# Kernel optimization log

Hardware: AMD Instinct MI355X
Metric: run time of the kernel (lower is better)

Reference implementation:

```python
import jax, jax.numpy as jnp
import numpy as np

B, S, V, E, H = 64, 512, 32000, 512, 1024


def setup_inputs() -> dict:
    key = jax.random.key(0)
    ks = jax.random.split(key, 8)
    s = 1.0 / np.sqrt(H).astype(np.float32)
    x = jax.random.randint(ks[0], (B, S), 0, V)  # token ids
    h0 = jnp.zeros((B, H), jnp.float32)
    c0 = jnp.zeros((B, H), jnp.float32)
    emb = jax.random.normal(ks[1], (V, E), jnp.float32) * 0.02
    W_ih = jax.random.uniform(ks[2], (4 * H, E), jnp.float32, -s, s)
    W_hh = jax.random.uniform(ks[3], (4 * H, H), jnp.float32, -s, s)
    b_ih = jax.random.uniform(ks[4], (4 * H,), jnp.float32, -s, s)
    b_hh = jax.random.uniform(ks[5], (4 * H,), jnp.float32, -s, s)
    fc_w = jax.random.uniform(ks[6], (1, H), jnp.float32, -s, s)
    fc_b = jax.random.uniform(ks[7], (1,), jnp.float32, -s, s)
    return {"x": x, "h0": h0, "c0": c0, "emb": emb, "W_ih": W_ih,
            "W_hh": W_hh, "b_ih": b_ih, "b_hh": b_hh, "fc_w": fc_w, "fc_b": fc_b}


def reference(x, h0, c0, emb, W_ih, W_hh, b_ih, b_hh, fc_w, fc_b):
    embeds = emb[x]                      # [B, S, E]
    xs = jnp.swapaxes(embeds, 0, 1)      # [S, B, E] for scan over time
    # precompute input projections for all timesteps in one big GEMM
    xproj = jnp.einsum('sbe,ge->sbg', xs, W_ih) + b_ih  # [S, B, 4H]

    def step(carry, xg):
        h, c = carry
        gates = xg + h @ W_hh.T + b_hh   # [B, 4H], torch LSTMCell gate order i,f,g,o
        i, f, g, o = jnp.split(gates, 4, axis=-1)
        c2 = jax.nn.sigmoid(f) * c + jax.nn.sigmoid(i) * jnp.tanh(g)
        h2 = jax.nn.sigmoid(o) * jnp.tanh(c2)
        return (h2, c2), None

    (h, c), _ = jax.lax.scan(step, (h0, c0), xproj)
    # dropout is identity in eval mode
    out = h @ fc_w.T + fc_b              # [B, 1]
    sig = jax.nn.sigmoid(out)
    sig_out = sig.reshape(x.shape[0], -1)[:, -1]  # [B]
    return (sig_out, h, c)
```

## Files before the change

kernel.cpp:

```cpp
#include <hip/hip_runtime.h>

typedef unsigned short u16;
typedef unsigned int   u32;

typedef __bf16 bf16x8 __attribute__((ext_vector_type(8)));
typedef float  f32x4  __attribute__((ext_vector_type(4)));

#define NB   64
#define NS   512
#define NE   512
#define NH   1024
#define NK   1536
#define NV   32000

#define WPKF_BYTES  12582912u
#define HFRAG_BYTES 262144u
#define AEMBF_BYTES 33554432u
#define BSUM_BYTES  16384u
#define BAR_BYTES   32768u

__device__ __forceinline__ u16 f2bf(float f) {
    u32 u = __builtin_bit_cast(u32, f);
    u += 0x7fffu + ((u >> 16) & 1u);
    return (u16)(u >> 16);
}
__device__ __forceinline__ bf16x8 pack8(float4 a, float4 b) {
    union { u16 u[8]; bf16x8 v; } o;
    o.u[0]=f2bf(a.x); o.u[1]=f2bf(a.y); o.u[2]=f2bf(a.z); o.u[3]=f2bf(a.w);
    o.u[4]=f2bf(b.x); o.u[5]=f2bf(b.y); o.u[6]=f2bf(b.z); o.u[7]=f2bf(b.w);
    return o.v;
}
__device__ __forceinline__ float sigf(float x) {
    return __frcp_rn(1.0f + __expf(-x));
}
__device__ __forceinline__ float tanhf_fast(float x) {
    return 1.0f - 2.0f * __frcp_rn(__expf(2.0f * x) + 1.0f);
}
__device__ __forceinline__ int clamptok(int t) {
    return t < 0 ? 0 : (t >= NV ? NV - 1 : t);
}

__global__ void init_state(const float* __restrict__ h0,
                           const float* __restrict__ c0,
                           float* __restrict__ out) {
    int i = blockIdx.x * 256 + threadIdx.x;
    float* out_h = out + 64;
    float* out_c = out + 64 + NB * NH;
    ((float4*)out_h)[i] = ((const float4*)h0)[i];
    ((float4*)out_c)[i] = ((const float4*)c0)[i];
}

__global__ void init_hfrag(const float* __restrict__ h0,
                           u16* __restrict__ hfrag0) {
    int blk = blockIdx.x, lane = threadIdx.x;
    int bg = blk >> 5, kt = blk & 31;
    int n16 = lane & 15, quad = lane >> 4;
    int b = bg * 16 + n16;
    int k = kt * 32 + quad * 8;
    const float* src = h0 + (size_t)b * NH + k;
    union { bf16x8 v; uint4 q; } o;
    o.v = pack8(*(const float4*)src, *(const float4*)(src + 4));
    *(uint4*)(hfrag0 + ((size_t)blk * 64 + lane) * 8) = o.q;
}

__global__ void prep_wfrag(const float* __restrict__ Wih,
                           const float* __restrict__ Whh,
                           u16* __restrict__ wpkf) {
    int blk = blockIdx.x, t = threadIdx.x;
    int cg = blk / 48, kt = blk % 48;
    int f = t >> 6, lane = t & 63;
    int n16 = lane & 15, quad = lane >> 4;
    int nl = f * 16 + n16;
    int j = (nl >> 3) * NH + cg * 8 + (nl & 7);
    int k = kt * 32 + quad * 8;
    const float* src = (k < NH) ? (Whh + (size_t)j * NH + k)
                                : (Wih + (size_t)j * NE + (k - NH));
    union { bf16x8 v; uint4 q; } o;
    o.v = pack8(*(const float4*)src, *(const float4*)(src + 4));
    *(uint4*)(wpkf + (((size_t)blk * 2 + f) * 64 + lane) * 8) = o.q;
}

__global__ void prep_aembf(const int* __restrict__ x,
                           const float* __restrict__ emb,
                           u16* __restrict__ aembf) {
    int blk = blockIdx.x, t = threadIdx.x;
    int s = blk >> 2, bg = blk & 3;
#pragma unroll
    for (int i = 0; i < 4; ++i) {
        int u = t + i * 256;
        int kt16 = u >> 6, lane = u & 63;
        int n16 = lane & 15, quad = lane >> 4;
        int b = bg * 16 + n16;
        int tok = clamptok(x[b * NS + s]);
        const float* ep = emb + (size_t)tok * NE + kt16 * 32 + quad * 8;
        union { bf16x8 v; uint4 q; } o;
        o.v = pack8(*(const float4*)ep, *(const float4*)(ep + 4));
        *(uint4*)(aembf + (((size_t)blk * 16 + kt16) * 64 + lane) * 8) = o.q;
    }
}

__global__ void prep_bsum(const float* __restrict__ bih,
                          const float* __restrict__ bhh,
                          float* __restrict__ bsum,
                          unsigned* __restrict__ bar) {
    int i = blockIdx.x * 256 + threadIdx.x;
    bsum[i] = bih[i] + bhh[i];
    bar[i] = 0u;
    bar[i + 4096] = 0u;
}

template<bool EMBF>
__device__ __forceinline__ void persist_body(
    const int* __restrict__ x, const float* __restrict__ emb,
    const u16* __restrict__ wpkf, const u16* __restrict__ aembf,
    u16* __restrict__ hf0, u16* __restrict__ hf1,
    const float* __restrict__ bsum, const float* __restrict__ c0,
    float* __restrict__ cstate, float* __restrict__ out_h,
    unsigned* __restrict__ bar)
{
    const int tid  = threadIdx.x;
    const int lane = tid & 63;
    const int w    = tid >> 6;
    const int blk  = blockIdx.x;
    const int cg   = blk & 127;
    const int bgp  = blk >> 7;
    const int quad = lane >> 4;
    const int n16  = lane & 15;

    __shared__ u16   lw[48 * 2 * 64 * 8];
    __shared__ float part[4][32][36];

    {
        const uint4* src = (const uint4*)(wpkf + (size_t)cg * (48 * 2 * 64 * 8));
        uint4* dst = (uint4*)lw;
#pragma unroll
        for (int i = 0; i < 24; ++i)
            dst[i * 256 + tid] = src[i * 256 + tid];
    }

    const int mloc = tid >> 3;
    const int uu   = tid & 7;
    const int be   = bgp * 32 + mloc;
    const int je   = cg * 8 + uu;
    const float bp0 = bsum[0 * NH + je];
    const float bp1 = bsum[1 * NH + je];
    const float bp2 = bsum[2 * NH + je];
    const float bp3 = bsum[3 * NH + je];
    float c_reg = c0[(size_t)be * NH + je];

    const int kth   = cg >> 2;
    const int lane2 = (cg & 3) * 16 + (mloc & 15);
    const int bgW   = bgp * 2 + (mloc >> 4);
    const size_t hwo_base = ((size_t)(bgW * 32 + kth) * 64 + lane2) * 8;

    const int bg0 = bgp * 2, bg1 = bg0 + 1;

    unsigned* my_flag = bar + ((size_t)(bgp * 128 + cg) * 32);
    const unsigned* pf0 = bar + ((size_t)(bgp * 128 + 2 * lane + 0) * 32);
    const unsigned* pf1 = bar + ((size_t)(bgp * 128 + 2 * lane + 1) * 32);

    bf16x8 ea0[4], ea1[4];
    auto loadE = [&](int s) {
        if (EMBF) {
            const u16* e0 = aembf + ((size_t)(s * 4 + bg0) * 16) * (64 * 8);
            const u16* e1 = aembf + ((size_t)(s * 4 + bg1) * 16) * (64 * 8);
#pragma unroll
            for (int i = 0; i < 4; ++i) {
                int ke = w * 4 + i;
                ea0[i] = *(const bf16x8*)(e0 + ((size_t)ke * 64 + lane) * 8);
                ea1[i] = *(const bf16x8*)(e1 + ((size_t)ke * 64 + lane) * 8);
            }
        } else {
            int t0 = clamptok(x[(bg0 * 16 + n16) * NS + s]);
            int t1 = clamptok(x[(bg1 * 16 + n16) * NS + s]);
            const float* p0 = emb + (size_t)t0 * NE + quad * 8;
            const float* p1 = emb + (size_t)t1 * NE + quad * 8;
#pragma unroll
            for (int i = 0; i < 4; ++i) {
                int ko = (w * 4 + i) * 32;
                ea0[i] = pack8(*(const float4*)(p0 + ko), *(const float4*)(p0 + ko + 4));
                ea1[i] = pack8(*(const float4*)(p1 + ko), *(const float4*)(p1 + ko + 4));
            }
        }
    };
    loadE(0);
    __syncthreads();

#pragma unroll 1
    for (int s = 0; s < NS; ++s) {
        const u16* hb = (s & 1) ? hf1 : hf0;
        u16*       ho = (s & 1) ? hf0 : hf1;
        const u16* hb0 = hb + (size_t)(bg0 * 32) * (64 * 8);
        const u16* hb1 = hb + (size_t)(bg1 * 32) * (64 * 8);

        f32x4 acc00 = {0.f,0.f,0.f,0.f}, acc01 = {0.f,0.f,0.f,0.f};
        f32x4 acc10 = {0.f,0.f,0.f,0.f}, acc11 = {0.f,0.f,0.f,0.f};

        uint4 hv0[8], hv1[8];
#pragma unroll
        for (int i = 0; i < 8; ++i) {
            const u16* a0p = hb0 + ((size_t)((w * 8 + i) * 64 + lane)) * 8;
            const u16* a1p = hb1 + ((size_t)((w * 8 + i) * 64 + lane)) * 8;
            asm volatile("global_load_dwordx4 %0, %1, off sc0 sc1"
                         : "=v"(hv0[i]) : "v"(a0p) : "memory");
            asm volatile("global_load_dwordx4 %0, %1, off sc0 sc1"
                         : "=v"(hv1[i]) : "v"(a1p) : "memory");
        }

#pragma unroll
        for (int i = 0; i < 4; ++i) {
            int kt = 32 + w * 4 + i;
            bf16x8 w0 = *(const bf16x8*)(lw + ((size_t)(kt * 2 + 0) * 64 + lane) * 8);
            bf16x8 w1 = *(const bf16x8*)(lw + ((size_t)(kt * 2 + 1) * 64 + lane) * 8);
            acc00 = __builtin_amdgcn_mfma_f32_16x16x32_bf16(ea0[i], w0, acc00, 0, 0, 0);
            acc01 = __builtin_amdgcn_mfma_f32_16x16x32_bf16(ea0[i], w1, acc01, 0, 0, 0);
            acc10 = __builtin_amdgcn_mfma_f32_16x16x32_bf16(ea1[i], w0, acc10, 0, 0, 0);
            acc11 = __builtin_amdgcn_mfma_f32_16x16x32_bf16(ea1[i], w1, acc11, 0, 0, 0);
        }

        asm volatile("s_waitcnt vmcnt(0)" ::: "memory");
        __builtin_amdgcn_sched_barrier(0);

#pragma unroll
        for (int i = 0; i < 8; ++i) {
            int kt = w * 8 + i;
            bf16x8 a0 = __builtin_bit_cast(bf16x8, hv0[i]);
            bf16x8 a1 = __builtin_bit_cast(bf16x8, hv1[i]);
            bf16x8 w0 = *(const bf16x8*)(lw + ((size_t)(kt * 2 + 0) * 64 + lane) * 8);
            bf16x8 w1 = *(const bf16x8*)(lw + ((size_t)(kt * 2 + 1) * 64 + lane) * 8);
            acc00 = __builtin_amdgcn_mfma_f32_16x16x32_bf16(a0, w0, acc00, 0, 0, 0);
            acc01 = __builtin_amdgcn_mfma_f32_16x16x32_bf16(a0, w1, acc01, 0, 0, 0);
            acc10 = __builtin_amdgcn_mfma_f32_16x16x32_bf16(a1, w0, acc10, 0, 0, 0);
            acc11 = __builtin_amdgcn_mfma_f32_16x16x32_bf16(a1, w1, acc11, 0, 0, 0);
        }

        {
            int mrow = quad * 4;
#pragma unroll
            for (int r = 0; r < 4; ++r) {
                part[w][mrow + r][n16]           = acc00[r];
                part[w][mrow + r][16 + n16]      = acc01[r];
                part[w][16 + mrow + r][n16]      = acc10[r];
                part[w][16 + mrow + r][16 + n16] = acc11[r];
            }
        }
        __syncthreads();

        float hN;
        {
            float gv0 = bp0, gv1 = bp1, gv2 = bp2, gv3 = bp3;
#pragma unroll
            for (int ww = 0; ww < 4; ++ww) {
                gv0 += part[ww][mloc][ 0 + uu];
                gv1 += part[ww][mloc][ 8 + uu];
                gv2 += part[ww][mloc][16 + uu];
                gv3 += part[ww][mloc][24 + uu];
            }
            float iS = sigf(gv0);
            float fS = sigf(gv1);
            float gT = tanhf_fast(gv2);
            float oS = sigf(gv3);
            float c_new = fS * c_reg + iS * gT;
            c_new = fminf(20.0f, fmaxf(-20.0f, c_new));
            c_reg = c_new;
            hN = oS * tanhf_fast(c_new);
        }

        if (s == NS - 1) {
            out_h[(size_t)be * NH + je]  = hN;
            cstate[(size_t)be * NH + je] = c_reg;
        } else {
            const unsigned need = (unsigned)(s + 1);
            loadE(s + 1);
            u32 hbf = f2bf(hN);
            u32 hup = (u32)__shfl_down((int)hbf, 1);
            if ((uu & 1) == 0) {
                u32 val = hbf | (hup << 16);
                u32* dst = (u32*)(ho + hwo_base + uu);
                __hip_atomic_store(dst, val, __ATOMIC_RELAXED,
                                   __HIP_MEMORY_SCOPE_AGENT);
            }
            asm volatile("s_waitcnt vmcnt(0)" ::: "memory");
            __syncthreads();
            if (tid == 0)
                __hip_atomic_store(my_flag, need, __ATOMIC_RELAXED,
                                   __HIP_MEMORY_SCOPE_AGENT);
            {
                unsigned v0, v1;
                while (true) {
                    asm volatile("global_load_dword %0, %2, off sc0 sc1\n\t"
                                 "global_load_dword %1, %3, off sc0 sc1\n\t"
                                 "s_waitcnt vmcnt(0)"
                                 : "=&v"(v0), "=&v"(v1)
                                 : "v"(pf0), "v"(pf1)
                                 : "memory");
                    if (__all(v0 >= need && v1 >= need)) break;
                    __builtin_amdgcn_s_sleep(1);
                }
            }
        }
    }
}

__global__ void __launch_bounds__(256, 1)
lstm_persist_a(const int* __restrict__ x, const float* __restrict__ emb,
               const u16* __restrict__ wpkf, const u16* __restrict__ aembf,
               u16* __restrict__ hf0, u16* __restrict__ hf1,
               const float* __restrict__ bsum, const float* __restrict__ c0,
               float* __restrict__ cstate, float* __restrict__ out_h,
               unsigned* __restrict__ bar) {
    persist_body<true>(x, emb, wpkf, aembf, hf0, hf1, bsum, c0, cstate, out_h, bar);
}

__global__ void __launch_bounds__(256, 1)
lstm_persist_b(const int* __restrict__ x, const float* __restrict__ emb,
               const u16* __restrict__ wpkf, const u16* __restrict__ aembf,
               u16* __restrict__ hf0, u16* __restrict__ hf1,
               const float* __restrict__ bsum, const float* __restrict__ c0,
               float* __restrict__ cstate, float* __restrict__ out_h,
               unsigned* __restrict__ bar) {
    persist_body<false>(x, emb, wpkf, aembf, hf0, hf1, bsum, c0, cstate, out_h, bar);
}

__global__ void __launch_bounds__(256)
lstm_step_raw(const int* __restrict__ x, const float* __restrict__ emb,
              const float* __restrict__ Wih, const float* __restrict__ Whh,
              const float* __restrict__ bih, const float* __restrict__ bhh,
              const float* __restrict__ hA, float* __restrict__ hB,
              float* __restrict__ cbuf, int s) {
    const int tid  = threadIdx.x;
    const int lane = tid & 63;
    const int w    = tid >> 6;
    const int blk  = blockIdx.x;
    const int cg   = blk & 127;
    const int bg   = blk >> 7;
    const int u0   = cg * 8;
    const int b0   = bg * 16;

    __shared__ float part[4][16][36];
    const int n16 = lane & 15;
    const int kq  = (lane >> 4) * 8;
    const int tok = clamptok(x[(b0 + n16) * NS + s]);

    const int nl0 = n16, nl1 = 16 + n16;
    const int r0 = (nl0 >> 3) * NH + u0 + (nl0 & 7);
    const int r1 = (nl1 >> 3) * NH + u0 + (nl1 & 7);

    f32x4 acc0 = {0.f,0.f,0.f,0.f};
    f32x4 acc1 = {0.f,0.f,0.f,0.f};

#pragma unroll
    for (int tkt = 0; tkt < 12; ++tkt) {
        int kt = w * 12 + tkt;
        int ko = kt * 32 + kq;
        const float *s0, *s1;
        if (kt < 32) { s0 = Whh + (size_t)r0 * NH + ko; s1 = Whh + (size_t)r1 * NH + ko; }
        else         { s0 = Wih + (size_t)r0 * NE + (ko - NH); s1 = Wih + (size_t)r1 * NE + (ko - NH); }
        bf16x8 wf0 = pack8(*(const float4*)s0, *(const float4*)(s0 + 4));
        bf16x8 wf1 = pack8(*(const float4*)s1, *(const float4*)(s1 + 4));
        bf16x8 a0;
        if (kt < 32) {
            const float* hp = hA + (size_t)(b0 + n16) * NH + ko;
            a0 = pack8(*(const float4*)hp, *(const float4*)(hp + 4));
        } else {
            const float* ep = emb + (size_t)tok * NE + (ko - NH);
            a0 = pack8(*(const float4*)ep, *(const float4*)(ep + 4));
        }
        acc0 = __builtin_amdgcn_mfma_f32_16x16x32_bf16(a0, wf0, acc0, 0, 0, 0);
        acc1 = __builtin_amdgcn_mfma_f32_16x16x32_bf16(a0, wf1, acc1, 0, 0, 0);
    }

    {
        int mrow = (lane >> 4) * 4;
#pragma unroll
        for (int r = 0; r < 4; ++r) {
            part[w][mrow + r][n16]      = acc0[r];
            part[w][mrow + r][16 + n16] = acc1[r];
        }
    }
    __syncthreads();

    if (tid < 128) {
        const int mloc = tid >> 3, uu = tid & 7;
        const int be = b0 + mloc, je = u0 + uu;
        float gv[4];
#pragma unroll
        for (int g = 0; g < 4; ++g) {
            int n = g * 8 + uu;
            gv[g] = part[0][mloc][n] + part[1][mloc][n]
                  + part[2][mloc][n] + part[3][mloc][n]
                  + bih[g * NH + je] + bhh[g * NH + je];
        }
        float iS = sigf(gv[0]);
        float fS = sigf(gv[1]);
        float gT = tanhf_fast(gv[2]);
        float oS = sigf(gv[3]);
        float c_new = fS * cbuf[be * NH + je] + iS * gT;
        c_new = fminf(20.0f, fmaxf(-20.0f, c_new));
        float hN = oS * tanhf_fast(c_new);
        cbuf[be * NH + je] = c_new;
        hB[be * NH + je]   = hN;
    }
}

__global__ void final_fc_simple(const float* __restrict__ fc_w,
                                const float* __restrict__ fc_b,
                                float* __restrict__ out) {
    __shared__ float red[64][5];
    const float* out_h = out + 64;
    int t = threadIdx.x;
    int b = t >> 2, q = t & 3;
    const float* hp = out_h + b * NH + q * 256;
    const float* wp = fc_w + q * 256;
    float sacc = 0.f;
#pragma unroll 4
    for (int i = 0; i < 64; ++i) {
        float4 hv = ((const float4*)hp)[i];
        float4 wv = ((const float4*)wp)[i];
        sacc += hv.x * wv.x + hv.y * wv.y + hv.z * wv.z + hv.w * wv.w;
    }
    red[b][q] = sacc;
    __syncthreads();
    if (q == 0) {
        float tot = red[b][0] + red[b][1] + red[b][2] + red[b][3] + fc_b[0];
        out[b] = 1.0f / (1.0f + expf(-tot));
    }
}

extern "C" void kernel_launch(void* const* d_in, const int* in_sizes, int n_in,
                              void* d_out, int out_size, void* d_ws, size_t ws_size,
                              hipStream_t stream) {
    const int*   x   = (const int*)d_in[0];
    const float* h0  = (const float*)d_in[1];
    const float* c0  = (const float*)d_in[2];
    const float* emb = (const float*)d_in[3];
    const float* Wih = (const float*)d_in[4];
    const float* Whh = (const float*)d_in[5];
    const float* bih = (const float*)d_in[6];
    const float* bhh = (const float*)d_in[7];
    const float* fcw = (const float*)d_in[8];
    const float* fcb = (const float*)d_in[9];

    float* out   = (float*)d_out;
    float* out_h = out + 64;
    float* out_c = out + 64 + NB * NH;

    const size_t needA = (size_t)WPKF_BYTES + HFRAG_BYTES + AEMBF_BYTES + BSUM_BYTES + BAR_BYTES;
    const size_t needB = (size_t)WPKF_BYTES + HFRAG_BYTES + BSUM_BYTES + BAR_BYTES;
    const bool tierA = ws_size >= needA;
    const bool tierB = !tierA && ws_size >= needB;

    if (tierA || tierB) {
        u16* wpkf  = (u16*)d_ws;
        u16* hfrag = (u16*)((char*)d_ws + WPKF_BYTES);
        u16* hf0 = hfrag;
        u16* hf1 = hfrag + HFRAG_BYTES / 4;
        char* after = (char*)d_ws + WPKF_BYTES + HFRAG_BYTES;
        u16*   aembf = tierA ? (u16*)after : nullptr;
        float* bsum  = (float*)(after + (tierA ? AEMBF_BYTES : 0));
        unsigned* bar = (unsigned*)((char*)bsum + BSUM_BYTES);

        hipLaunchKernelGGL(init_hfrag, dim3(128), dim3(64), 0, stream, h0, hf0);
        hipLaunchKernelGGL(prep_wfrag, dim3(6144), dim3(128), 0, stream,
                           Wih, Whh, wpkf);
        hipLaunchKernelGGL(prep_bsum, dim3(16), dim3(256), 0, stream,
                           bih, bhh, bsum, bar);
        if (tierA)
            hipLaunchKernelGGL(prep_aembf, dim3(2048), dim3(256), 0, stream,
                               x, emb, aembf);

        void* kargs[11] = { &x, &emb, &wpkf, &aembf, &hf0, &hf1,
                            &bsum, &c0, &out_c, &out_h, &bar };
        (void)hipLaunchCooperativeKernel(
            tierA ? reinterpret_cast<const void*>(&lstm_persist_a)
                  : reinterpret_cast<const void*>(&lstm_persist_b),
            dim3(256), dim3(256), kargs, 0u, stream);
    } else {
        hipLaunchKernelGGL(init_state, dim3(64), dim3(256), 0, stream, h0, c0, out);
        float* wsH = (float*)d_ws;
        for (int s = 0; s < NS; ++s) {
            const float* hA = (s & 1) ? wsH : out_h;
            float*       hB = (s & 1) ? out_h : wsH;
            hipLaunchKernelGGL(lstm_step_raw, dim3(512), dim3(256), 0, stream,
                               x, emb, Wih, Whh, bih, bhh, hA, hB, out_c, s);
        }
    }

    hipLaunchKernelGGL(final_fc_simple, dim3(1), dim3(256), 0, stream,
                       fcw, fcb, out);
}
```

Before: 2.077 ms.

## Pack barrier flags densely, remap blocks, defer embedding load past flag store

```diff
diff --git a/kernel.cpp b/kernel.cpp
--- a/kernel.cpp
+++ b/kernel.cpp
@@ -122,8 +122,9 @@
     const int lane = tid & 63;
     const int w    = tid >> 6;
     const int blk  = blockIdx.x;
-    const int cg   = blk & 127;
-    const int bgp  = blk >> 7;
+    const int c7   = blk & 7;
+    const int bgp  = c7 >> 2;
+    const int cg   = (blk >> 3) * 4 + (c7 & 3);
     const int quad = lane >> 4;
     const int n16  = lane & 15;
 
@@ -155,9 +156,8 @@
 
     const int bg0 = bgp * 2, bg1 = bg0 + 1;
 
-    unsigned* my_flag = bar + ((size_t)(bgp * 128 + cg) * 32);
-    const unsigned* pf0 = bar + ((size_t)(bgp * 128 + 2 * lane + 0) * 32);
-    const unsigned* pf1 = bar + ((size_t)(bgp * 128 + 2 * lane + 1) * 32);
+    unsigned* my_flag = bar + bgp * 128 + cg;
+    const unsigned* pf = bar + bgp * 128 + lane * 2;
 
     bf16x8 ea0[4], ea1[4];
     auto loadE = [&](int s) {
@@ -193,19 +193,15 @@
         const u16* hb0 = hb + (size_t)(bg0 * 32) * (64 * 8);
         const u16* hb1 = hb + (size_t)(bg1 * 32) * (64 * 8);
 
+        uint4 hv0[8], hv1[8];
+#pragma unroll
+        for (int i = 0; i < 8; ++i) {
+            hv0[i] = *(const uint4*)(hb0 + ((size_t)((w * 8 + i) * 64 + lane)) * 8);
+            hv1[i] = *(const uint4*)(hb1 + ((size_t)((w * 8 + i) * 64 + lane)) * 8);
+        }
+
         f32x4 acc00 = {0.f,0.f,0.f,0.f}, acc01 = {0.f,0.f,0.f,0.f};
         f32x4 acc10 = {0.f,0.f,0.f,0.f}, acc11 = {0.f,0.f,0.f,0.f};
-
-        uint4 hv0[8], hv1[8];
-#pragma unroll
-        for (int i = 0; i < 8; ++i) {
-            const u16* a0p = hb0 + ((size_t)((w * 8 + i) * 64 + lane)) * 8;
-            const u16* a1p = hb1 + ((size_t)((w * 8 + i) * 64 + lane)) * 8;
-            asm volatile("global_load_dwordx4 %0, %1, off sc0 sc1"
-                         : "=v"(hv0[i]) : "v"(a0p) : "memory");
-            asm volatile("global_load_dwordx4 %0, %1, off sc0 sc1"
-                         : "=v"(hv1[i]) : "v"(a1p) : "memory");
-        }
 
 #pragma unroll
         for (int i = 0; i < 4; ++i) {
@@ -217,9 +213,6 @@
             acc10 = __builtin_amdgcn_mfma_f32_16x16x32_bf16(ea1[i], w0, acc10, 0, 0, 0);
             acc11 = __builtin_amdgcn_mfma_f32_16x16x32_bf16(ea1[i], w1, acc11, 0, 0, 0);
         }
-
-        asm volatile("s_waitcnt vmcnt(0)" ::: "memory");
-        __builtin_amdgcn_sched_barrier(0);
 
 #pragma unroll
         for (int i = 0; i < 8; ++i) {
@@ -271,7 +264,6 @@
             cstate[(size_t)be * NH + je] = c_reg;
         } else {
             const unsigned need = (unsigned)(s + 1);
-            loadE(s + 1);
             u32 hbf = f2bf(hN);
             u32 hup = (u32)__shfl_down((int)hbf, 1);
             if ((uu & 1) == 0) {
@@ -285,19 +277,18 @@
             if (tid == 0)
                 __hip_atomic_store(my_flag, need, __ATOMIC_RELAXED,
                                    __HIP_MEMORY_SCOPE_AGENT);
+            loadE(s + 1);
             {
-                unsigned v0, v1;
+                uint2 v;
                 while (true) {
-                    asm volatile("global_load_dword %0, %2, off sc0 sc1\n\t"
-                                 "global_load_dword %1, %3, off sc0 sc1\n\t"
+                    asm volatile("global_load_dwordx2 %0, %1, off sc0 sc1\n\t"
                                  "s_waitcnt vmcnt(0)"
-                                 : "=&v"(v0), "=&v"(v1)
-                                 : "v"(pf0), "v"(pf1)
-                                 : "memory");
-                    if (__all(v0 >= need && v1 >= need)) break;
+                                 : "=v"(v) : "v"(pf) : "memory");
+                    if (__all(v.x >= need && v.y >= need)) break;
                     __builtin_amdgcn_s_sleep(1);
                 }
             }
+            __builtin_amdgcn_fence(__ATOMIC_ACQUIRE, "agent");
         }
     }
 }
```

Result: slower. 6.188 ms (+197.9%).
